# Optimization experiments

Measured on AMD Instinct MI355X. Metric: run time of the kernel, lower is better.

Reference implementation:

```python
import jax, jax.numpy as jnp
import numpy as np

D_NODE, C, N_HEAD = 256, 32, 8
N_SEQ, N_RES = 256, 256
LN_EPS = 1e-5
MASK_BIAS = 1e9


def setup_inputs() -> dict:
    key = jax.random.key(0)
    ks = jax.random.split(key, 4)
    return {
        "M_raw": jax.random.normal(ks[0], (N_SEQ, N_RES, D_NODE), dtype=jnp.float32),
        "M_mask": jnp.ones((N_SEQ, N_RES), dtype=jnp.float32),
        "ln_w": jnp.ones((D_NODE,), jnp.float32),
        "ln_b": jnp.zeros((D_NODE,), jnp.float32),
        "qkv_w": jax.random.normal(ks[1], (D_NODE, 3 * N_HEAD * C), jnp.float32) * (D_NODE ** -0.5),
        "gate_w": jax.random.normal(ks[2], (D_NODE, N_HEAD * C), jnp.float32) * (D_NODE ** -0.5),
        "gate_b": jnp.ones((N_HEAD * C,), jnp.float32),
        "out_w": jax.random.normal(ks[3], (N_HEAD * C, D_NODE), jnp.float32) * ((N_HEAD * C) ** -0.5),
        "out_b": jnp.zeros((D_NODE,), jnp.float32),
    }


def reference(M_raw, M_mask, ln_w, ln_b, qkv_w, gate_w, gate_b, out_w, out_b):
    # Transpose to column-attention layout: [N_res, N_seq, d]
    M = jnp.swapaxes(M_raw, -2, -3)
    mask = jnp.swapaxes(M_mask, -1, -2)  # [N_res, N_seq]

    # LayerNorm over feature dim
    mu = jnp.mean(M, axis=-1, keepdims=True)
    var = jnp.mean(jnp.square(M - mu), axis=-1, keepdims=True)
    Mn = (M - mu) * jax.lax.rsqrt(var + LN_EPS) * ln_w + ln_b

    # QKV projection (no bias), split heads
    r, s = Mn.shape[0], Mn.shape[1]
    qkv = (Mn @ qkv_w).reshape(r, s, 3, N_HEAD, C)
    q, k, v = qkv[:, :, 0], qkv[:, :, 1], qkv[:, :, 2]  # [r, s, h, c]
    q = q * (C ** -0.5)

    # Masked attention over the sequence (column) axis
    logits = jnp.einsum('rqhc,rkhc->rhqk', q, k)
    logits = logits + (MASK_BIAS * (mask - 1.0))[:, None, None, :]
    weights = jax.nn.softmax(logits, axis=-1)
    o = jnp.einsum('rhqk,rkhc->rqhc', weights, v).reshape(r, s, N_HEAD * C)

    # Sigmoid gating and output projection
    gate = jax.nn.sigmoid(Mn @ gate_w + gate_b)
    out = (o * gate) @ out_w + out_b

    # Residual in original layout
    return M_raw + jnp.swapaxes(out, -2, -3)
```

## Files before the change

kernel.cpp:

```cpp
#include <hip/hip_runtime.h>


typedef short bf16x8 __attribute__((ext_vector_type(8)));
typedef float f32x4  __attribute__((ext_vector_type(4)));

union U8 { uint w[4]; bf16x8 v; ushort u[8]; };

__device__ __forceinline__ ushort f2bf(float f) {
  uint u = __float_as_uint(f);
  u = (u + 0x7fffu + ((u >> 16) & 1u)) >> 16;
  return (ushort)u;
}

__device__ __forceinline__ uint pk2(float lo, float hi) {
  return (uint)f2bf(lo) | ((uint)f2bf(hi) << 16);
}

__device__ __forceinline__ f32x4 MFMA(bf16x8 a, bf16x8 b, f32x4 c) {
  return __builtin_amdgcn_mfma_f32_16x16x32_bf16(a, b, c, 0, 0, 0);
}

__device__ __forceinline__ bf16x8 ldG(const ushort* __restrict__ p, int row, int ko) {
  return *(const bf16x8*)(p + (size_t)row * 256 + ko);
}

__global__ __launch_bounds__(256) void k_prep(const float* __restrict__ qkv_w,
                                              const float* __restrict__ gate_w,
                                              const float* __restrict__ out_w,
                                              ushort* __restrict__ ws) {
  __shared__ ushort t[64][72];
  const int b = blockIdx.x;
  const float* src; ushort* dst; int C, r0, c0; bool scale_q = false;
  if (b < 48)      { src = qkv_w;  dst = ws;          C = 768; r0 = (b/12)*64;      c0 = (b%12)*64; scale_q = true; }
  else if (b < 64) { int bb = b-48; src = gate_w; dst = ws + 196608; C = 256; r0 = (bb>>2)*64; c0 = (bb&3)*64; }
  else             { int bb = b-64; src = out_w;  dst = ws + 262144; C = 256; r0 = (bb>>2)*64; c0 = (bb&3)*64; }
  const int tid = threadIdx.x;
  const int cc = tid & 63, rb = tid >> 6;
  #pragma unroll
  for (int j = 0; j < 16; ++j) {
    const int rr = j*4 + rb;
    float v = src[(size_t)(r0+rr)*C + c0 + cc];
    if (scale_q && (c0+cc) < 256) v *= 0.17677669529663687f;
    t[cc][rr] = f2bf(v);
  }
  __syncthreads();
  const int dd = (tid & 31)*2, cb = tid >> 5;
  #pragma unroll
  for (int j = 0; j < 8; ++j) {
    const int c2 = j*8 + cb;
    const uint wv = (uint)t[c2][dd] | ((uint)t[c2][dd+1] << 16);
    *(uint*)(dst + (size_t)(c0+c2)*256 + r0 + dd) = wv;
  }
}

__global__ __launch_bounds__(512, 2) void k_attn(
    const float* __restrict__ M_raw, const float* __restrict__ M_mask,
    const float* __restrict__ ln_w, const float* __restrict__ ln_b,
    const ushort* __restrict__ qkv_wT, const ushort* __restrict__ gate_wT,
    const float* __restrict__ gate_b, ushort* __restrict__ og)
{
  extern __shared__ char smem[];
  const int r    = blockIdx.x;
  const int tid  = threadIdx.x;
  const int w    = tid >> 6;
  const int lane = tid & 63;
  const int l15  = lane & 15;
  const int g    = lane >> 4;
  const int Q0   = w << 5;
  const int swz  = (l15 & 3) << 4;
  const f32x4 Z  = {0.f, 0.f, 0.f, 0.f};

  bf16x8 mn[2][8];
  #pragma unroll
  for (int mt = 0; mt < 2; ++mt) {
    const int s = Q0 + mt*16 + l15;
    const float* rowp = M_raw + (size_t)s * 65536 + (size_t)r * 256;
    float4 xa[8], xb[8];
    float sum = 0.f, sq = 0.f;
    #pragma unroll
    for (int kk = 0; kk < 8; ++kk) {
      xa[kk] = *(const float4*)(rowp + kk*32 + g*8);
      xb[kk] = *(const float4*)(rowp + kk*32 + g*8 + 4);
      sum += xa[kk].x + xa[kk].y + xa[kk].z + xa[kk].w
           + xb[kk].x + xb[kk].y + xb[kk].z + xb[kk].w;
      sq  += xa[kk].x*xa[kk].x + xa[kk].y*xa[kk].y + xa[kk].z*xa[kk].z + xa[kk].w*xa[kk].w
           + xb[kk].x*xb[kk].x + xb[kk].y*xb[kk].y + xb[kk].z*xb[kk].z + xb[kk].w*xb[kk].w;
    }
    sum += __shfl_xor(sum, 16, 64);  sum += __shfl_xor(sum, 32, 64);
    sq  += __shfl_xor(sq,  16, 64);  sq  += __shfl_xor(sq,  32, 64);
    const float mu = sum * 0.00390625f;
    const float rs = rsqrtf(sq * 0.00390625f - mu*mu + 1e-5f);
    #pragma unroll
    for (int kk = 0; kk < 8; ++kk) {
      const float4 wa = *(const float4*)(ln_w + kk*32 + g*8);
      const float4 wb = *(const float4*)(ln_w + kk*32 + g*8 + 4);
      const float4 ba = *(const float4*)(ln_b + kk*32 + g*8);
      const float4 bb = *(const float4*)(ln_b + kk*32 + g*8 + 4);
      U8 u;
      u.w[0] = pk2((xa[kk].x-mu)*rs*wa.x+ba.x, (xa[kk].y-mu)*rs*wa.y+ba.y);
      u.w[1] = pk2((xa[kk].z-mu)*rs*wa.z+ba.z, (xa[kk].w-mu)*rs*wa.w+ba.w);
      u.w[2] = pk2((xb[kk].x-mu)*rs*wb.x+bb.x, (xb[kk].y-mu)*rs*wb.y+bb.y);
      u.w[3] = pk2((xb[kk].z-mu)*rs*wb.z+bb.z, (xb[kk].w-mu)*rs*wb.w+bb.w);
      mn[mt][kk] = u.v;
    }
  }

  uint mb0 = 0, mb1 = 0;
  for (int i = 0; i < 64; ++i) {
    const int k = ((i >> 2) << 4) + (g << 2) + (i & 3);
    const uint bit = (M_mask[(size_t)k * 256 + r] > 0.5f) ? 1u : 0u;
    if (i < 32) mb0 |= bit << i; else mb1 |= bit << (i - 32);
  }

  auto projT = [&](const ushort* __restrict__ W, int rowbase, f32x4 (&acc)[2][2]) {
    #pragma unroll
    for (int mtc = 0; mtc < 2; ++mtc) {
      #pragma unroll
      for (int kk = 0; kk < 8; ++kk) {
        const bf16x8 a = ldG(W, rowbase + mtc*16 + l15, kk*32 + g*8);
        acc[mtc][0] = MFMA(a, mn[0][kk], acc[mtc][0]);
        acc[mtc][1] = MFMA(a, mn[1][kk], acc[mtc][1]);
      }
    }
  };
  auto projV = [&](const ushort* __restrict__ W, int rowbase, f32x4 (&acc)[2][2]) {
    #pragma unroll
    for (int ntc = 0; ntc < 2; ++ntc) {
      #pragma unroll
      for (int kk = 0; kk < 8; ++kk) {
        const bf16x8 bfr = ldG(W, rowbase + ntc*16 + l15, kk*32 + g*8);
        acc[0][ntc] = MFMA(mn[0][kk], bfr, acc[0][ntc]);
        acc[1][ntc] = MFMA(mn[1][kk], bfr, acc[1][ntc]);
      }
    }
  };

  f32x4 kaT[2][2] = {{Z,Z},{Z,Z}}, vaN[2][2] = {{Z,Z},{Z,Z}};
  projT(qkv_wT, 256 + 0, kaT);
  projV(qkv_wT, 512 + 0, vaN);

  for (int h = 0; h < 8; ++h) {
    const int hs = h << 5;
    const int kO = (h & 1) * 16384;
    const int vO = 32768 + (h & 1) * 16384;

    #pragma unroll
    for (int mtc = 0; mtc < 2; ++mtc)
      #pragma unroll
      for (int nts = 0; nts < 2; ++nts) {
        uint2 p2; p2.x = pk2(kaT[mtc][nts][0], kaT[mtc][nts][1]);
                  p2.y = pk2(kaT[mtc][nts][2], kaT[mtc][nts][3]);
        const int s = Q0 + nts*16 + l15;
        *(uint2*)(smem + kO + s*64 + ((mtc*32 + g*8) ^ swz)) = p2;
      }
    #pragma unroll
    for (int mt = 0; mt < 2; ++mt)
      #pragma unroll
      for (int ntc = 0; ntc < 2; ++ntc) {
        uint2 p2; p2.x = pk2(vaN[mt][ntc][0], vaN[mt][ntc][1]);
                  p2.y = pk2(vaN[mt][ntc][2], vaN[mt][ntc][3]);
        const int c = ntc*16 + l15;
        *(uint2*)(smem + vO + c*512 + (((Q0 + mt*16 + g*4)*2) ^ ((c & 7) << 4))) = p2;
      }

    f32x4 qaT[2][2] = {{Z,Z},{Z,Z}};
    projT(qkv_wT, hs, qaT);
    #pragma unroll
    for (int mtc = 0; mtc < 2; ++mtc)
      #pragma unroll
      for (int nts = 0; nts < 2; ++nts) {
        uint2 p2; p2.x = pk2(qaT[mtc][nts][0], qaT[mtc][nts][1]);
                  p2.y = pk2(qaT[mtc][nts][2], qaT[mtc][nts][3]);
        const int s = Q0 + nts*16 + l15;
        *(uint2*)(smem + 65536 + s*64 + ((mtc*32 + g*8) ^ swz)) = p2;
      }
    __syncthreads();
    const bf16x8 bq0 = *(const bf16x8*)(smem + 65536 + (Q0 + l15)*64      + ((g*16) ^ swz));
    const bf16x8 bq1 = *(const bf16x8*)(smem + 65536 + (Q0 + 16 + l15)*64 + ((g*16) ^ swz));

    __syncthreads();

    f32x4 S[16][2];
    #pragma unroll
    for (int mt = 0; mt < 16; ++mt) { S[mt][0] = Z; S[mt][1] = Z; }
    #pragma unroll
    for (int kt = 0; kt < 16; ++kt) {
      const bf16x8 ak = *(const bf16x8*)(smem + kO + (kt*16 + l15)*64 + ((g*16) ^ swz));
      S[kt][0] = MFMA(ak, bq0, S[kt][0]);
      S[kt][1] = MFMA(ak, bq1, S[kt][1]);
    }

    float inv0 = 0.f, inv1 = 0.f;
    uint pkk[2][16][2];
    #pragma unroll
    for (int nt = 0; nt < 2; ++nt) {
      float mx = -3.0e38f;
      #pragma unroll
      for (int mt = 0; mt < 16; ++mt)
        #pragma unroll
        for (int i = 0; i < 4; ++i) mx = fmaxf(mx, S[mt][nt][i]);
      mx = fmaxf(mx, __shfl_xor(mx, 16, 64));
      mx = fmaxf(mx, __shfl_xor(mx, 32, 64));
      float sum = 0.f;
      #pragma unroll
      for (int mt = 0; mt < 16; ++mt)
        #pragma unroll
        for (int i = 0; i < 4; ++i) {
          float p = __expf(S[mt][nt][i] - mx);
          const int bi = mt*4 + i;
          const uint bit = (bi < 32) ? (mb0 >> bi) : (mb1 >> (bi - 32));
          p = (bit & 1u) ? p : 0.f;
          S[mt][nt][i] = p;
          sum += p;
        }
      sum += __shfl_xor(sum, 16, 64);
      sum += __shfl_xor(sum, 32, 64);
      const float iv = 1.0f / sum;
      if (nt == 0) inv0 = iv; else inv1 = iv;
      #pragma unroll
      for (int mt = 0; mt < 16; ++mt) {
        pkk[nt][mt][0] = pk2(S[mt][nt][0], S[mt][nt][1]);
        pkk[nt][mt][1] = pk2(S[mt][nt][2], S[mt][nt][3]);
      }
    }

    f32x4 oA[2][2] = {{Z,Z},{Z,Z}};
    const int srcA = l15 + 32*(g & 1);
    const int srcB = srcA + 16;
    const bool hi = (g >= 2);
    #pragma unroll
    for (int kb = 0; kb < 8; ++kb) {
      U8 bp[2];
      #pragma unroll
      for (int nt = 0; nt < 2; ++nt) {
        const uint a0 = __shfl(pkk[nt][2*kb][0],   srcA), b0 = __shfl(pkk[nt][2*kb+1][0], srcA);
        const uint a1 = __shfl(pkk[nt][2*kb][1],   srcA), b1 = __shfl(pkk[nt][2*kb+1][1], srcA);
        const uint a2 = __shfl(pkk[nt][2*kb][0],   srcB), b2 = __shfl(pkk[nt][2*kb+1][0], srcB);
        const uint a3 = __shfl(pkk[nt][2*kb][1],   srcB), b3 = __shfl(pkk[nt][2*kb+1][1], srcB);
        bp[nt].w[0] = hi ? b0 : a0;  bp[nt].w[1] = hi ? b1 : a1;
        bp[nt].w[2] = hi ? b2 : a2;  bp[nt].w[3] = hi ? b3 : a3;
      }
      #pragma unroll
      for (int mtc = 0; mtc < 2; ++mtc) {
        const int c = mtc*16 + l15;
        const bf16x8 av = *(const bf16x8*)(smem + vO + c*512 + ((kb*64 + g*16) ^ ((c & 7) << 4)));
        oA[mtc][0] = MFMA(av, bp[0].v, oA[mtc][0]);
        oA[mtc][1] = MFMA(av, bp[1].v, oA[mtc][1]);
      }
    }

    if (h < 7) {
      #pragma unroll
      for (int a = 0; a < 2; ++a)
        #pragma unroll
        for (int bb = 0; bb < 2; ++bb) { kaT[a][bb] = Z; vaN[a][bb] = Z; }
      projT(qkv_wT, 256 + hs + 32, kaT);
      projV(qkv_wT, 512 + hs + 32, vaN);
    }

    f32x4 gaT[2][2] = {{Z,Z},{Z,Z}};
    projT(gate_wT, hs, gaT);
    #pragma unroll
    for (int mtc = 0; mtc < 2; ++mtc)
      #pragma unroll
      for (int nt = 0; nt < 2; ++nt) {
        float vals[4];
        #pragma unroll
        for (int i = 0; i < 4; ++i) {
          const float gb  = gate_b[hs + mtc*16 + g*4 + i];
          const float sig = 1.0f / (1.0f + __expf(-(gaT[mtc][nt][i] + gb)));
          vals[i] = oA[mtc][nt][i] * (nt ? inv1 : inv0) * sig;
        }
        uint2 p2; p2.x = pk2(vals[0], vals[1]); p2.y = pk2(vals[2], vals[3]);
        const int s = Q0 + nt*16 + l15;
        *(uint2*)(smem + 65536 + s*64 + ((mtc*32 + g*8) ^ swz)) = p2;
      }
    __syncthreads();
    uint* ogw = (uint*)og;
    const size_t ob = ((size_t)(r*8 + h) * 256) * 16;
    #pragma unroll
    for (int j2 = 0; j2 < 8; ++j2) {
      const int lin = j2*64 + lane;
      const int row = Q0 + (lin >> 4);
      const int cu  = lin & 15;
      const uint wv = *(const uint*)(smem + 65536 + row*64 + ((cu*4) ^ ((row & 3) << 4)));
      ogw[ob + (size_t)row*16 + cu] = wv;
    }
  }
}

__global__ __launch_bounds__(256) void k_out(
    const ushort* __restrict__ og, const ushort* __restrict__ out_wT,
    const float* __restrict__ out_b, const float* __restrict__ M_raw,
    float* __restrict__ out)
{
  const int blk  = blockIdx.x;
  const int tid  = threadIdx.x;
  const int w    = tid >> 6;
  const int lane = tid & 63;
  const int l15  = lane & 15;
  const int g    = lane >> 4;
  const int row0 = blk * 64 + w * 16;
  const int r    = row0 >> 8;
  const int s0   = row0 & 255;

  const f32x4 Z = {0.f, 0.f, 0.f, 0.f};
  f32x4 acc[16];
  #pragma unroll
  for (int nt = 0; nt < 16; ++nt) acc[nt] = Z;

  #pragma unroll
  for (int kk = 0; kk < 8; ++kk) {
    const bf16x8 a = *(const bf16x8*)(og + ((size_t)(r*8 + kk)*256 + s0 + l15)*32 + g*8);
    #pragma unroll
    for (int nt = 0; nt < 16; ++nt) {
      const bf16x8 b = ldG(out_wT, nt*16 + l15, kk*32 + g*8);
      acc[nt] = MFMA(a, b, acc[nt]);
    }
  }

  #pragma unroll
  for (int nt = 0; nt < 16; ++nt) {
    const int d = nt*16 + l15;
    const float ob = out_b[d];
    #pragma unroll
    for (int i = 0; i < 4; ++i) {
      const int s = s0 + 4*g + i;
      const size_t idx = (size_t)s * 65536 + (size_t)r * 256 + d;
      out[idx] = M_raw[idx] + acc[nt][i] + ob;
    }
  }
}

extern "C" void kernel_launch(void* const* d_in, const int* in_sizes, int n_in,
                              void* d_out, int out_size, void* d_ws, size_t ws_size,
                              hipStream_t stream) {
  const float* M_raw  = (const float*)d_in[0];
  const float* M_mask = (const float*)d_in[1];
  const float* ln_w   = (const float*)d_in[2];
  const float* ln_b   = (const float*)d_in[3];
  const float* qkv_w  = (const float*)d_in[4];
  const float* gate_w = (const float*)d_in[5];
  const float* gate_b = (const float*)d_in[6];
  const float* out_w  = (const float*)d_in[7];
  const float* out_b  = (const float*)d_in[8];

  ushort* ws      = (ushort*)d_ws;
  ushort* qkv_wT  = ws;
  ushort* gate_wT = ws + 196608;
  ushort* out_wT  = ws + 262144;
  ushort* og      = ws + 327680;

  hipFuncSetAttribute(reinterpret_cast<const void*>(k_attn),
                      hipFuncAttributeMaxDynamicSharedMemorySize, 81920);

  hipLaunchKernelGGL(k_prep, dim3(80), dim3(256), 0, stream, qkv_w, gate_w, out_w, ws);
  hipLaunchKernelGGL(k_attn, dim3(256), dim3(512), 81920, stream,
                     M_raw, M_mask, ln_w, ln_b, qkv_wT, gate_wT, gate_b, og);
  hipLaunchKernelGGL(k_out, dim3(1024), dim3(256), 0, stream,
                     og, out_wT, out_b, M_raw, (float*)d_out);
}
```

Measured before the change: 376.6 us.

## Rewrite column attention kernel around 32x32x16 MFMA tiles with register-resident Q

The attention kernel moves from 16x16x32 to 32x32x16 bf16 MFMA tiles. Each wave now owns 32 query rows laid out for the larger tile. Q operands are rebuilt in registers through cross-half-wave shuffles instead of a round trip through LDS, and softmax probabilities are packed the same way. A fast path skips masking when the whole mask is ones. Shared memory is shrunk and re-laid out with padded strides, the next head's K/V/Q projection overlaps the current head's output, and one barrier per head is removed. This risks higher register pressure from the 16-wide accumulators, which at 512 threads with two blocks per SM could cause spills.

```diff
diff --git a/kernel.cpp b/kernel.cpp
--- a/kernel.cpp
+++ b/kernel.cpp
@@ -3,6 +3,7 @@
 
 typedef short bf16x8 __attribute__((ext_vector_type(8)));
 typedef float f32x4  __attribute__((ext_vector_type(4)));
+typedef float f32x16 __attribute__((ext_vector_type(16)));
 
 union U8 { uint w[4]; bf16x8 v; ushort u[8]; };
 
@@ -16,12 +17,22 @@
   return (uint)f2bf(lo) | ((uint)f2bf(hi) << 16);
 }
 
-__device__ __forceinline__ f32x4 MFMA(bf16x8 a, bf16x8 b, f32x4 c) {
+__device__ __forceinline__ f32x16 MFMA32(bf16x8 a, bf16x8 b, f32x16 c) {
+  return __builtin_amdgcn_mfma_f32_32x32x16_bf16(a, b, c, 0, 0, 0);
+}
+__device__ __forceinline__ f32x4 MFMA16(bf16x8 a, bf16x8 b, f32x4 c) {
   return __builtin_amdgcn_mfma_f32_16x16x32_bf16(a, b, c, 0, 0, 0);
 }
 
-__device__ __forceinline__ bf16x8 ldG(const ushort* __restrict__ p, int row, int ko) {
+__device__ __forceinline__ bf16x8 ldG8(const ushort* __restrict__ p, int row, int ko) {
   return *(const bf16x8*)(p + (size_t)row * 256 + ko);
+}
+
+__device__ __forceinline__ f32x16 zero16() {
+  f32x16 z;
+  #pragma unroll
+  for (int i = 0; i < 16; ++i) z[i] = 0.f;
+  return z;
 }
 
 __global__ __launch_bounds__(256) void k_prep(const float* __restrict__ qkv_w,
@@ -53,6 +64,10 @@
   }
 }
 
+#define KOFF 0
+#define VOFF 20480
+#define GOFF 37376
+
 __global__ __launch_bounds__(512, 2) void k_attn(
     const float* __restrict__ M_raw, const float* __restrict__ M_mask,
     const float* __restrict__ ln_w, const float* __restrict__ ln_b,
@@ -64,227 +79,197 @@
   const int tid  = threadIdx.x;
   const int w    = tid >> 6;
   const int lane = tid & 63;
-  const int l15  = lane & 15;
-  const int g    = lane >> 4;
+  const int l31  = lane & 31;
+  const int hl   = lane >> 5;
   const int Q0   = w << 5;
-  const int swz  = (l15 & 3) << 4;
-  const f32x4 Z  = {0.f, 0.f, 0.f, 0.f};
-
-  bf16x8 mn[2][8];
-  #pragma unroll
-  for (int mt = 0; mt < 2; ++mt) {
-    const int s = Q0 + mt*16 + l15;
-    const float* rowp = M_raw + (size_t)s * 65536 + (size_t)r * 256;
-    float4 xa[8], xb[8];
-    float sum = 0.f, sq = 0.f;
-    #pragma unroll
-    for (int kk = 0; kk < 8; ++kk) {
-      xa[kk] = *(const float4*)(rowp + kk*32 + g*8);
-      xb[kk] = *(const float4*)(rowp + kk*32 + g*8 + 4);
-      sum += xa[kk].x + xa[kk].y + xa[kk].z + xa[kk].w
-           + xb[kk].x + xb[kk].y + xb[kk].z + xb[kk].w;
-      sq  += xa[kk].x*xa[kk].x + xa[kk].y*xa[kk].y + xa[kk].z*xa[kk].z + xa[kk].w*xa[kk].w
-           + xb[kk].x*xb[kk].x + xb[kk].y*xb[kk].y + xb[kk].z*xb[kk].z + xb[kk].w*xb[kk].w;
-    }
-    sum += __shfl_xor(sum, 16, 64);  sum += __shfl_xor(sum, 32, 64);
-    sq  += __shfl_xor(sq,  16, 64);  sq  += __shfl_xor(sq,  32, 64);
-    const float mu = sum * 0.00390625f;
-    const float rs = rsqrtf(sq * 0.00390625f - mu*mu + 1e-5f);
-    #pragma unroll
-    for (int kk = 0; kk < 8; ++kk) {
-      const float4 wa = *(const float4*)(ln_w + kk*32 + g*8);
-      const float4 wb = *(const float4*)(ln_w + kk*32 + g*8 + 4);
-      const float4 ba = *(const float4*)(ln_b + kk*32 + g*8);
-      const float4 bb = *(const float4*)(ln_b + kk*32 + g*8 + 4);
-      U8 u;
-      u.w[0] = pk2((xa[kk].x-mu)*rs*wa.x+ba.x, (xa[kk].y-mu)*rs*wa.y+ba.y);
-      u.w[1] = pk2((xa[kk].z-mu)*rs*wa.z+ba.z, (xa[kk].w-mu)*rs*wa.w+ba.w);
-      u.w[2] = pk2((xb[kk].x-mu)*rs*wb.x+bb.x, (xb[kk].y-mu)*rs*wb.y+bb.y);
-      u.w[3] = pk2((xb[kk].z-mu)*rs*wb.z+bb.z, (xb[kk].w-mu)*rs*wb.w+bb.w);
-      mn[mt][kk] = u.v;
-    }
-  }
-
-  uint mb0 = 0, mb1 = 0;
-  for (int i = 0; i < 64; ++i) {
-    const int k = ((i >> 2) << 4) + (g << 2) + (i & 3);
-    const uint bit = (M_mask[(size_t)k * 256 + r] > 0.5f) ? 1u : 0u;
-    if (i < 32) mb0 |= bit << i; else mb1 |= bit << (i - 32);
-  }
-
-  auto projT = [&](const ushort* __restrict__ W, int rowbase, f32x4 (&acc)[2][2]) {
-    #pragma unroll
-    for (int mtc = 0; mtc < 2; ++mtc) {
+  const int s    = Q0 + l31;
+
+  const float* rowp = M_raw + (size_t)s * 65536 + (size_t)r * 256;
+  float4 xa[16], xb[16];
+  float sum = 0.f, sq = 0.f;
+  #pragma unroll
+  for (int dt = 0; dt < 16; ++dt) {
+    xa[dt] = *(const float4*)(rowp + dt*16 + hl*8);
+    xb[dt] = *(const float4*)(rowp + dt*16 + hl*8 + 4);
+    sum += xa[dt].x + xa[dt].y + xa[dt].z + xa[dt].w
+         + xb[dt].x + xb[dt].y + xb[dt].z + xb[dt].w;
+    sq  += xa[dt].x*xa[dt].x + xa[dt].y*xa[dt].y + xa[dt].z*xa[dt].z + xa[dt].w*xa[dt].w
+         + xb[dt].x*xb[dt].x + xb[dt].y*xb[dt].y + xb[dt].z*xb[dt].z + xb[dt].w*xb[dt].w;
+  }
+  sum += __shfl_xor(sum, 32, 64);
+  sq  += __shfl_xor(sq,  32, 64);
+  const float mu = sum * 0.00390625f;
+  const float rs = rsqrtf(sq * 0.00390625f - mu*mu + 1e-5f);
+  bf16x8 mn[16];
+  #pragma unroll
+  for (int dt = 0; dt < 16; ++dt) {
+    const float4 wa = *(const float4*)(ln_w + dt*16 + hl*8);
+    const float4 wb = *(const float4*)(ln_w + dt*16 + hl*8 + 4);
+    const float4 ba = *(const float4*)(ln_b + dt*16 + hl*8);
+    const float4 bb = *(const float4*)(ln_b + dt*16 + hl*8 + 4);
+    U8 u;
+    u.w[0] = pk2((xa[dt].x-mu)*rs*wa.x+ba.x, (xa[dt].y-mu)*rs*wa.y+ba.y);
+    u.w[1] = pk2((xa[dt].z-mu)*rs*wa.z+ba.z, (xa[dt].w-mu)*rs*wa.w+ba.w);
+    u.w[2] = pk2((xb[dt].x-mu)*rs*wb.x+bb.x, (xb[dt].y-mu)*rs*wb.y+bb.y);
+    u.w[3] = pk2((xb[dt].z-mu)*rs*wb.z+bb.z, (xb[dt].w-mu)*rs*wb.w+bb.w);
+    mn[dt] = u.v;
+  }
+
+  uint m0=0, m1=0, m2=0, m3=0;
+  for (int b = 0; b < 32; ++b) {
+    const int k0 = ((b>>4)<<5) + (b&3) + (((b>>2)&3)<<3) + hl*4;
+    m0 |= (M_mask[(size_t)(k0      )*256 + r] > 0.5f ? 1u:0u) << b;
+    m1 |= (M_mask[(size_t)(k0 +  64)*256 + r] > 0.5f ? 1u:0u) << b;
+    m2 |= (M_mask[(size_t)(k0 + 128)*256 + r] > 0.5f ? 1u:0u) << b;
+    m3 |= (M_mask[(size_t)(k0 + 192)*256 + r] > 0.5f ? 1u:0u) << b;
+  }
+  const bool full = ((m0 & m1 & m2 & m3) == 0xFFFFFFFFu);
+
+  auto mergeOp = [&](float q0, float q1, float q2, float q3,
+                     float q4, float q5, float q6, float q7) -> bf16x8 {
+    const uint x0 = pk2(q0, q1), x1 = pk2(q2, q3);
+    const uint z0 = pk2(q4, q5), z1 = pk2(q6, q7);
+    const uint xx0 = __shfl_xor(x0, 32, 64), xx1 = __shfl_xor(x1, 32, 64);
+    const uint zz0 = __shfl_xor(z0, 32, 64), zz1 = __shfl_xor(z1, 32, 64);
+    U8 u;
+    u.w[0] = hl ? zz0 : x0;
+    u.w[1] = hl ? zz1 : x1;
+    u.w[2] = hl ? z0  : xx0;
+    u.w[3] = hl ? z1  : xx1;
+    return u.v;
+  };
+
+  auto projT = [&](const ushort* __restrict__ W, int rowbase) -> f32x16 {
+    f32x16 acc = zero16();
+    #pragma unroll
+    for (int dt = 0; dt < 16; ++dt)
+      acc = MFMA32(ldG8(W, rowbase + l31, dt*16 + hl*8), mn[dt], acc);
+    return acc;
+  };
+  auto projN = [&](const ushort* __restrict__ W, int rowbase) -> f32x16 {
+    f32x16 acc = zero16();
+    #pragma unroll
+    for (int dt = 0; dt < 16; ++dt)
+      acc = MFMA32(mn[dt], ldG8(W, rowbase + l31, dt*16 + hl*8), acc);
+    return acc;
+  };
+  auto packB = [&](const f32x16& q, bf16x8& lo, bf16x8& hi2) {
+    lo  = mergeOp(q[0], q[1], q[2],  q[3],  q[4],  q[5],  q[6],  q[7]);
+    hi2 = mergeOp(q[8], q[9], q[10], q[11], q[12], q[13], q[14], q[15]);
+  };
+  auto stageKV = [&](const f32x16& KA, const f32x16& VA) {
+    #pragma unroll
+    for (int rq = 0; rq < 4; ++rq) {
+      uint2 p2;
+      p2.x = pk2(KA[4*rq],   KA[4*rq+1]);
+      p2.y = pk2(KA[4*rq+2], KA[4*rq+3]);
+      *(uint2*)(smem + KOFF + s*80 + rq*16 + hl*8) = p2;
+      p2.x = pk2(VA[4*rq],   VA[4*rq+1]);
+      p2.y = pk2(VA[4*rq+2], VA[4*rq+3]);
+      *(uint2*)(smem + VOFF + l31*528 + Q0*2 + rq*16 + hl*8) = p2;
+    }
+  };
+
+  bf16x8 bq0, bq1;
+  {
+    f32x16 KA = projT(qkv_wT, 256 + 0);
+    f32x16 VA = projN(qkv_wT, 512 + 0);
+    stageKV(KA, VA);
+    f32x16 QA = projT(qkv_wT, 0);
+    packB(QA, bq0, bq1);
+  }
+  __syncthreads();
+
+  for (int hd = 0; hd < 8; ++hd) {
+    const int hs = hd << 5;
+
+    f32x16 S[8];
+    #pragma unroll
+    for (int kt = 0; kt < 8; ++kt) {
+      const bf16x8 a0 = *(const bf16x8*)(smem + KOFF + (kt*32 + l31)*80 + hl*16);
+      const bf16x8 a1 = *(const bf16x8*)(smem + KOFF + (kt*32 + l31)*80 + 32 + hl*16);
+      f32x16 t = MFMA32(a0, bq0, zero16());
+      S[kt] = MFMA32(a1, bq1, t);
+    }
+
+    float mx = -3.0e38f;
+    #pragma unroll
+    for (int kt = 0; kt < 8; ++kt)
       #pragma unroll
-      for (int kk = 0; kk < 8; ++kk) {
-        const bf16x8 a = ldG(W, rowbase + mtc*16 + l15, kk*32 + g*8);
-        acc[mtc][0] = MFMA(a, mn[0][kk], acc[mtc][0]);
-        acc[mtc][1] = MFMA(a, mn[1][kk], acc[mtc][1]);
-      }
-    }
-  };
-  auto projV = [&](const ushort* __restrict__ W, int rowbase, f32x4 (&acc)[2][2]) {
-    #pragma unroll
-    for (int ntc = 0; ntc < 2; ++ntc) {
+      for (int i = 0; i < 16; ++i) mx = fmaxf(mx, S[kt][i]);
+    mx = fmaxf(mx, __shfl_xor(mx, 32, 64));
+    float sm = 0.f;
+    if (full) {
       #pragma unroll
-      for (int kk = 0; kk < 8; ++kk) {
-        const bf16x8 bfr = ldG(W, rowbase + ntc*16 + l15, kk*32 + g*8);
-        acc[0][ntc] = MFMA(mn[0][kk], bfr, acc[0][ntc]);
-        acc[1][ntc] = MFMA(mn[1][kk], bfr, acc[1][ntc]);
-      }
-    }
-  };
-
-  f32x4 kaT[2][2] = {{Z,Z},{Z,Z}}, vaN[2][2] = {{Z,Z},{Z,Z}};
-  projT(qkv_wT, 256 + 0, kaT);
-  projV(qkv_wT, 512 + 0, vaN);
-
-  for (int h = 0; h < 8; ++h) {
-    const int hs = h << 5;
-    const int kO = (h & 1) * 16384;
-    const int vO = 32768 + (h & 1) * 16384;
-
-    #pragma unroll
-    for (int mtc = 0; mtc < 2; ++mtc)
+      for (int kt = 0; kt < 8; ++kt)
+        #pragma unroll
+        for (int i = 0; i < 16; ++i) { const float p = __expf(S[kt][i] - mx); S[kt][i] = p; sm += p; }
+    } else {
+      const uint mm[4] = {m0, m1, m2, m3};
       #pragma unroll
-      for (int nts = 0; nts < 2; ++nts) {
-        uint2 p2; p2.x = pk2(kaT[mtc][nts][0], kaT[mtc][nts][1]);
-                  p2.y = pk2(kaT[mtc][nts][2], kaT[mtc][nts][3]);
-        const int s = Q0 + nts*16 + l15;
-        *(uint2*)(smem + kO + s*64 + ((mtc*32 + g*8) ^ swz)) = p2;
-      }
-    #pragma unroll
-    for (int mt = 0; mt < 2; ++mt)
-      #pragma unroll
-      for (int ntc = 0; ntc < 2; ++ntc) {
-        uint2 p2; p2.x = pk2(vaN[mt][ntc][0], vaN[mt][ntc][1]);
-                  p2.y = pk2(vaN[mt][ntc][2], vaN[mt][ntc][3]);
-        const int c = ntc*16 + l15;
-        *(uint2*)(smem + vO + c*512 + (((Q0 + mt*16 + g*4)*2) ^ ((c & 7) << 4))) = p2;
-      }
-
-    f32x4 qaT[2][2] = {{Z,Z},{Z,Z}};
-    projT(qkv_wT, hs, qaT);
-    #pragma unroll
-    for (int mtc = 0; mtc < 2; ++mtc)
-      #pragma unroll
-      for (int nts = 0; nts < 2; ++nts) {
-        uint2 p2; p2.x = pk2(qaT[mtc][nts][0], qaT[mtc][nts][1]);
-                  p2.y = pk2(qaT[mtc][nts][2], qaT[mtc][nts][3]);
-        const int s = Q0 + nts*16 + l15;
-        *(uint2*)(smem + 65536 + s*64 + ((mtc*32 + g*8) ^ swz)) = p2;
-      }
+      for (int kt = 0; kt < 8; ++kt)
+        #pragma unroll
+        for (int i = 0; i < 16; ++i) {
+          const int bi = kt*16 + i;
+          float p = __expf(S[kt][i] - mx);
+          p = ((mm[bi>>5] >> (bi & 31)) & 1u) ? p : 0.f;
+          S[kt][i] = p; sm += p;
+        }
+    }
+    sm += __shfl_xor(sm, 32, 64);
+    const float inv = 1.0f / sm;
+
+    f32x16 O = zero16();
+    #pragma unroll
+    for (int kt = 0; kt < 8; ++kt) {
+      const bf16x8 pa0 = mergeOp(S[kt][0]*inv,  S[kt][1]*inv,  S[kt][2]*inv,  S[kt][3]*inv,
+                                 S[kt][4]*inv,  S[kt][5]*inv,  S[kt][6]*inv,  S[kt][7]*inv);
+      const bf16x8 vb0 = *(const bf16x8*)(smem + VOFF + l31*528 + kt*64 + hl*16);
+      O = MFMA32(pa0, vb0, O);
+      const bf16x8 pa1 = mergeOp(S[kt][8]*inv,  S[kt][9]*inv,  S[kt][10]*inv, S[kt][11]*inv,
+                                 S[kt][12]*inv, S[kt][13]*inv, S[kt][14]*inv, S[kt][15]*inv);
+      const bf16x8 vb1 = *(const bf16x8*)(smem + VOFF + l31*528 + kt*64 + 32 + hl*16);
+      O = MFMA32(pa1, vb1, O);
+    }
+
+    f32x16 G = projN(gate_wT, hs);
+    const float gb = gate_b[hs + l31];
+    #pragma unroll
+    for (int rq = 0; rq < 4; ++rq) {
+      float v0 = O[4*rq+0] / (1.f + __expf(-(G[4*rq+0] + gb)));
+      float v1 = O[4*rq+1] / (1.f + __expf(-(G[4*rq+1] + gb)));
+      float v2 = O[4*rq+2] / (1.f + __expf(-(G[4*rq+2] + gb)));
+      float v3 = O[4*rq+3] / (1.f + __expf(-(G[4*rq+3] + gb)));
+      *(uint*)(smem + GOFF + ((Q0>>1) + rq*4 + hl*2 + 0)*128 + l31*4) = pk2(v0, v1);
+      *(uint*)(smem + GOFF + ((Q0>>1) + rq*4 + hl*2 + 1)*128 + l31*4) = pk2(v2, v3);
+    }
+
+    f32x16 KAn, VAn;
+    if (hd < 7) {
+      KAn = projT(qkv_wT, 256 + hs + 32);
+      VAn = projN(qkv_wT, 512 + hs + 32);
+    }
+
     __syncthreads();
-    const bf16x8 bq0 = *(const bf16x8*)(smem + 65536 + (Q0 + l15)*64      + ((g*16) ^ swz));
-    const bf16x8 bq1 = *(const bf16x8*)(smem + 65536 + (Q0 + 16 + l15)*64 + ((g*16) ^ swz));
-
-    __syncthreads();
-
-    f32x4 S[16][2];
-    #pragma unroll
-    for (int mt = 0; mt < 16; ++mt) { S[mt][0] = Z; S[mt][1] = Z; }
-    #pragma unroll
-    for (int kt = 0; kt < 16; ++kt) {
-      const bf16x8 ak = *(const bf16x8*)(smem + kO + (kt*16 + l15)*64 + ((g*16) ^ swz));
-      S[kt][0] = MFMA(ak, bq0, S[kt][0]);
-      S[kt][1] = MFMA(ak, bq1, S[kt][1]);
-    }
-
-    float inv0 = 0.f, inv1 = 0.f;
-    uint pkk[2][16][2];
-    #pragma unroll
-    for (int nt = 0; nt < 2; ++nt) {
-      float mx = -3.0e38f;
-      #pragma unroll
-      for (int mt = 0; mt < 16; ++mt)
-        #pragma unroll
-        for (int i = 0; i < 4; ++i) mx = fmaxf(mx, S[mt][nt][i]);
-      mx = fmaxf(mx, __shfl_xor(mx, 16, 64));
-      mx = fmaxf(mx, __shfl_xor(mx, 32, 64));
-      float sum = 0.f;
-      #pragma unroll
-      for (int mt = 0; mt < 16; ++mt)
-        #pragma unroll
-        for (int i = 0; i < 4; ++i) {
-          float p = __expf(S[mt][nt][i] - mx);
-          const int bi = mt*4 + i;
-          const uint bit = (bi < 32) ? (mb0 >> bi) : (mb1 >> (bi - 32));
-          p = (bit & 1u) ? p : 0.f;
-          S[mt][nt][i] = p;
-          sum += p;
-        }
-      sum += __shfl_xor(sum, 16, 64);
-      sum += __shfl_xor(sum, 32, 64);
-      const float iv = 1.0f / sum;
-      if (nt == 0) inv0 = iv; else inv1 = iv;
-      #pragma unroll
-      for (int mt = 0; mt < 16; ++mt) {
-        pkk[nt][mt][0] = pk2(S[mt][nt][0], S[mt][nt][1]);
-        pkk[nt][mt][1] = pk2(S[mt][nt][2], S[mt][nt][3]);
-      }
-    }
-
-    f32x4 oA[2][2] = {{Z,Z},{Z,Z}};
-    const int srcA = l15 + 32*(g & 1);
-    const int srcB = srcA + 16;
-    const bool hi = (g >= 2);
-    #pragma unroll
-    for (int kb = 0; kb < 8; ++kb) {
-      U8 bp[2];
-      #pragma unroll
-      for (int nt = 0; nt < 2; ++nt) {
-        const uint a0 = __shfl(pkk[nt][2*kb][0],   srcA), b0 = __shfl(pkk[nt][2*kb+1][0], srcA);
-        const uint a1 = __shfl(pkk[nt][2*kb][1],   srcA), b1 = __shfl(pkk[nt][2*kb+1][1], srcA);
-        const uint a2 = __shfl(pkk[nt][2*kb][0],   srcB), b2 = __shfl(pkk[nt][2*kb+1][0], srcB);
-        const uint a3 = __shfl(pkk[nt][2*kb][1],   srcB), b3 = __shfl(pkk[nt][2*kb+1][1], srcB);
-        bp[nt].w[0] = hi ? b0 : a0;  bp[nt].w[1] = hi ? b1 : a1;
-        bp[nt].w[2] = hi ? b2 : a2;  bp[nt].w[3] = hi ? b3 : a3;
-      }
-      #pragma unroll
-      for (int mtc = 0; mtc < 2; ++mtc) {
-        const int c = mtc*16 + l15;
-        const bf16x8 av = *(const bf16x8*)(smem + vO + c*512 + ((kb*64 + g*16) ^ ((c & 7) << 4)));
-        oA[mtc][0] = MFMA(av, bp[0].v, oA[mtc][0]);
-        oA[mtc][1] = MFMA(av, bp[1].v, oA[mtc][1]);
-      }
-    }
-
-    if (h < 7) {
-      #pragma unroll
-      for (int a = 0; a < 2; ++a)
-        #pragma unroll
-        for (int bb = 0; bb < 2; ++bb) { kaT[a][bb] = Z; vaN[a][bb] = Z; }
-      projT(qkv_wT, 256 + hs + 32, kaT);
-      projV(qkv_wT, 512 + hs + 32, vaN);
-    }
-
-    f32x4 gaT[2][2] = {{Z,Z},{Z,Z}};
-    projT(gate_wT, hs, gaT);
-    #pragma unroll
-    for (int mtc = 0; mtc < 2; ++mtc)
-      #pragma unroll
-      for (int nt = 0; nt < 2; ++nt) {
-        float vals[4];
-        #pragma unroll
-        for (int i = 0; i < 4; ++i) {
-          const float gb  = gate_b[hs + mtc*16 + g*4 + i];
-          const float sig = 1.0f / (1.0f + __expf(-(gaT[mtc][nt][i] + gb)));
-          vals[i] = oA[mtc][nt][i] * (nt ? inv1 : inv0) * sig;
-        }
-        uint2 p2; p2.x = pk2(vals[0], vals[1]); p2.y = pk2(vals[2], vals[3]);
-        const int s = Q0 + nt*16 + l15;
-        *(uint2*)(smem + 65536 + s*64 + ((mtc*32 + g*8) ^ swz)) = p2;
-      }
-    __syncthreads();
+
     uint* ogw = (uint*)og;
-    const size_t ob = ((size_t)(r*8 + h) * 256) * 16;
-    #pragma unroll
-    for (int j2 = 0; j2 < 8; ++j2) {
-      const int lin = j2*64 + lane;
-      const int row = Q0 + (lin >> 4);
-      const int cu  = lin & 15;
-      const uint wv = *(const uint*)(smem + 65536 + row*64 + ((cu*4) ^ ((row & 3) << 4)));
-      ogw[ob + (size_t)row*16 + cu] = wv;
+    const size_t ob = (size_t)(r*8 + hd) * 4096;
+    #pragma unroll
+    for (int j = 0; j < 8; ++j) {
+      const int sl   = j*4 + (lane >> 4);
+      const int srow = Q0 + sl;
+      const int cu   = lane & 15;
+      const uint2 u2 = *(const uint2*)(smem + GOFF + (srow>>1)*128 + cu*8);
+      const uint outv = (srow & 1) ? ((u2.x >> 16) | (u2.y & 0xFFFF0000u))
+                                   : ((u2.x & 0xFFFFu) | (u2.y << 16));
+      ogw[ob + (size_t)srow*16 + cu] = outv;
+    }
+
+    if (hd < 7) {
+      stageKV(KAn, VAn);
+      f32x16 QA = projT(qkv_wT, hs + 32);
+      packB(QA, bq0, bq1);
+      __syncthreads();
     }
   }
 }
@@ -314,8 +299,8 @@
     const bf16x8 a = *(const bf16x8*)(og + ((size_t)(r*8 + kk)*256 + s0 + l15)*32 + g*8);
     #pragma unroll
     for (int nt = 0; nt < 16; ++nt) {
-      const bf16x8 b = ldG(out_wT, nt*16 + l15, kk*32 + g*8);
-      acc[nt] = MFMA(a, b, acc[nt]);
+      const bf16x8 b = ldG8(out_wT, nt*16 + l15, kk*32 + g*8);
+      acc[nt] = MFMA16(a, b, acc[nt]);
     }
   }
 
@@ -325,8 +310,8 @@
     const float ob = out_b[d];
     #pragma unroll
     for (int i = 0; i < 4; ++i) {
-      const int s = s0 + 4*g + i;
-      const size_t idx = (size_t)s * 65536 + (size_t)r * 256 + d;
+      const int ss = s0 + 4*g + i;
+      const size_t idx = (size_t)ss * 65536 + (size_t)r * 256 + d;
       out[idx] = M_raw[idx] + acc[nt][i] + ob;
     }
   }
@@ -352,10 +337,10 @@
   ushort* og      = ws + 327680;
 
   hipFuncSetAttribute(reinterpret_cast<const void*>(k_attn),
-                      hipFuncAttributeMaxDynamicSharedMemorySize, 81920);
+                      hipFuncAttributeMaxDynamicSharedMemorySize, 53760);
 
   hipLaunchKernelGGL(k_prep, dim3(80), dim3(256), 0, stream, qkv_w, gate_w, out_w, ws);
-  hipLaunchKernelGGL(k_attn, dim3(256), dim3(512), 81920, stream,
+  hipLaunchKernelGGL(k_attn, dim3(256), dim3(512), 53760, stream,
                      M_raw, M_mask, ln_w, ln_b, qkv_wT, gate_wT, gate_b, og);
   hipLaunchKernelGGL(k_out, dim3(1024), dim3(256), 0, stream,
                      og, out_wT, out_b, M_raw, (float*)d_out);
```

Result: slower. 946.7 us (+151.4%).
